# Kernel optimization log

Hardware: AMD Instinct MI355X
Metric: run time of the kernel (lower is better)

Reference implementation:

```python
import jax, jax.numpy as jnp
import numpy as np

B, D_IN, H1, H2, A = 8192, 512, 4096, 4096, 64
QMIN, QMAX = -128.0, 127.0  # int8 saturation range


def _int_vals(key, shape, spread):
    # integer-valued fixed-point tensor stored as float32
    return jnp.clip(jnp.round(jax.random.normal(key, shape) * spread), QMIN * spread, QMAX * spread).astype(jnp.float32)


def setup_inputs() -> dict:
    key = jax.random.key(0)
    ks = jax.random.split(key, 9)
    x = jnp.clip(jnp.round(jax.random.normal(ks[0], (B, D_IN)) * 32.0), QMIN, QMAX).astype(jnp.float32)
    w1 = jnp.clip(jnp.round(jax.random.normal(ks[1], (H1, D_IN)) * 16.0), QMIN, QMAX).astype(jnp.float32)
    b1 = _int_vals(ks[2], (H1,), 256.0)
    w2 = jnp.clip(jnp.round(jax.random.normal(ks[3], (H2, H1)) * 16.0), QMIN, QMAX).astype(jnp.float32)
    b2 = _int_vals(ks[4], (H2,), 256.0)
    w_mu = jnp.clip(jnp.round(jax.random.normal(ks[5], (A, H2)) * 16.0), QMIN, QMAX).astype(jnp.float32)
    b_mu = _int_vals(ks[6], (A,), 256.0)
    w_prob = jnp.clip(jnp.round(jax.random.normal(ks[7], (A, H2)) * 16.0), QMIN, QMAX).astype(jnp.float32)
    b_prob = _int_vals(ks[8], (A,), 256.0)
    M = jnp.full((1,), 2.0 ** -10, dtype=jnp.float32)  # per-layer requant multiplier
    s = jnp.full((1,), 0.05, dtype=jnp.float32)        # activation quantize scale
    return {
        "x": x, "w1": w1, "b1": b1, "w2": w2, "b2": b2,
        "w_mu": w_mu, "b_mu": b_mu, "w_prob": w_prob, "b_prob": b_prob,
        "M1": M, "M2": M, "M_mu": M, "M_prob": M,
        "s2": s, "s_mu": s, "s_prob": s,
    }


def _qlinear(x, w, b, M):
    # genesys fixed-point linear: int accumulate then requantize by multiplier M
    acc = jnp.matmul(x, w.T) + b  # integer-valued fp32 accumulator
    return jnp.round(M * acc)


def _quantize(src, scale, zero_point=0.0):
    return jnp.clip(jnp.round(src / scale) + zero_point, QMIN, QMAX)


def reference(x, w1, b1, w2, b2, w_mu, b_mu, w_prob, b_prob, M1, M2, M_mu, M_prob, s2, s_mu, s_prob):
    h = jax.nn.relu(_qlinear(x, w1, b1, M1))
    h = _quantize(h, s2)
    h = jax.nn.relu(_qlinear(h, w2, b2, M2))
    # NOTE: original forward_int feeds the un-quantized relu output into the
    # heads (x_mu/x_prob quantizations are dead code) and returns only prob.
    prob = _qlinear(h, w_prob, b_prob, M_prob)
    return prob
```

## Files before the change

kernel.cpp:

```cpp
#include <hip/hip_runtime.h>
#include <stdint.h>

#define NB   8192
#define DIN  512
#define NH1  4096
#define NH2  4096
#define NA   64

typedef int v4i __attribute__((ext_vector_type(4)));

__device__ __forceinline__ v4i mfma_i8(v4i a, v4i b, v4i c) {
    return __builtin_amdgcn_mfma_i32_16x16x64_i8(a, b, c, 0, 0, 0);
}

__device__ __forceinline__ void gload16(const void* g, const void* l) {
    __builtin_amdgcn_global_load_lds(
        (const __attribute__((address_space(1))) void*)(uintptr_t)g,
        (__attribute__((address_space(3))) void*)(uint32_t)(uintptr_t)l,
        16, 0, 0);
}

__global__ __launch_bounds__(256)
void prep(const float* __restrict__ x,  const float* __restrict__ w1,
          const float* __restrict__ w2, const float* __restrict__ wp,
          signed char* __restrict__ xf, signed char* __restrict__ w1_i8,
          signed char* __restrict__ w2_i8, signed char* __restrict__ wp_i8,
          int* __restrict__ S)
{
    __shared__ int red[256];
    const int b   = blockIdx.x;
    const int tid = threadIdx.x;

    if (b < 18432) {
        const float* in  = (b < 16384) ? w2 : w1;
        signed char* out = (b < 16384) ? w2_i8 : w1_i8;
        const int i = ((b < 16384) ? b : (b - 16384)) * 256 + tid;
        const float4 v = ((const float4*)in)[i];
        char4 c;
        c.x = (signed char)__float2int_rn(v.x);
        c.y = (signed char)__float2int_rn(v.y);
        c.z = (signed char)__float2int_rn(v.z);
        c.w = (signed char)__float2int_rn(v.w);
        ((char4*)out)[i] = c;
    } else if (b < 19456) {
        const int u   = (b - 18432) * 256 + tid;
        const int g   = u >> 9;
        const int kt  = (u >> 6) & 7;
        const int l   = u & 63;
        const int row = g * 16 + (l & 15);
        const int k0  = kt * 64 + (l >> 4) * 16;
        const float4* src = (const float4*)(x + (size_t)row * DIN + k0);
        signed char v[16];
        #pragma unroll
        for (int q = 0; q < 4; ++q) {
            const float4 f = src[q];
            v[q*4+0] = (signed char)__float2int_rn(f.x);
            v[q*4+1] = (signed char)__float2int_rn(f.y);
            v[q*4+2] = (signed char)__float2int_rn(f.z);
            v[q*4+3] = (signed char)__float2int_rn(f.w);
        }
        *(int4*)(xf + (size_t)u * 16) = *(const int4*)v;
    } else if (b < 19712) {
        const int i = (b - 19456) * 256 + tid;
        const float4 v = ((const float4*)wp)[i];
        char4 c;
        c.x = (signed char)__float2int_rn(v.x);
        c.y = (signed char)__float2int_rn(v.y);
        c.z = (signed char)__float2int_rn(v.z);
        c.w = (signed char)__float2int_rn(v.w);
        ((char4*)wp_i8)[i] = c;
    } else {
        const int a = b - 19712;
        int p = 0;
        for (int k = tid; k < NH2; k += 256) p += __float2int_rn(wp[(size_t)a * NH2 + k]);
        red[tid] = p; __syncthreads();
        for (int s = 128; s > 0; s >>= 1) { if (tid < s) red[tid] += red[tid + s]; __syncthreads(); }
        if (tid == 0) S[a] = red[0];
    }
}

template <int EPI>
__global__ __launch_bounds__(512, 4)
void gemm_af(const signed char* __restrict__ Af,
             const signed char* __restrict__ Bg,
             int M, int N, int K,
             const float* __restrict__ bias,
             const float* __restrict__ Mscale,
             const float* __restrict__ qscale,
             signed char* __restrict__ out0,
             signed char* __restrict__ out1)
{
    __shared__ __align__(16) signed char lds[69632];

    const int tid  = threadIdx.x;
    const int lane = tid & 63;
    const int wid  = tid >> 6;
    const int wm   = wid >> 1, wn = wid & 1;

    const int nwg  = gridDim.x;
    const int bid  = blockIdx.x;
    const int swzb = (bid & 7) * (nwg >> 3) + (bid >> 3);
    const int nbx  = N >> 7;
    const int bx   = swzb % nbx;
    const int by   = swzb / nbx;
    const int bm0  = by << 8, bn0 = bx << 7;

    const int srow = tid >> 2;
    const int sc   = (((tid & 3) ^ ((tid >> 3) & 3)) << 4);
    const signed char* bS = Bg + (size_t)(bn0 + srow) * K + sc;

    const int r    = lane & 15;
    const int pc   = (((lane >> 4) ^ ((r >> 1) & 3)) << 4);
    const int boff = wn * 4096 + r * 64 + pc;

    const int NKT = K >> 6;
    const signed char* afB = Af + (((size_t)((bm0 >> 4) + wm * 4) * NKT) << 10) + lane * 16;

    const int nt = K >> 6;

    v4i af[4], bf[4];
    #pragma unroll
    for (int m = 0; m < 4; ++m)
        af[m] = *(const v4i*)(afB + (((size_t)(m * NKT)) << 10));
    gload16(bS,      lds + tid * 16);
    gload16(bS + 64, lds + 8192 + tid * 16);
    asm volatile("s_waitcnt vmcnt(1)" ::: "memory");
    __builtin_amdgcn_s_barrier();

    v4i acc[4][4] = {};

    for (int t = 0; t < nt; ++t) {
        const signed char* L = lds + (t % 3) * 8192;
        #pragma unroll
        for (int n = 0; n < 4; ++n) bf[n] = *(const v4i*)(L + boff + n * 1024);

        const size_t tl = (size_t)((t + 1 < nt) ? (t + 1) : t);

        __builtin_amdgcn_s_setprio(1);
        #pragma unroll
        for (int m = 0; m < 4; ++m) {
            #pragma unroll
            for (int n = 0; n < 4; ++n)
                acc[m][n] = mfma_i8(af[m], bf[n], acc[m][n]);
            af[m] = *(const v4i*)(afB + (((size_t)(m * NKT) + tl) << 10));
        }
        __builtin_amdgcn_s_setprio(0);

        if (t + 2 < nt) {
            gload16(bS + ((t + 2) << 6), lds + ((t + 2) % 3) * 8192 + tid * 16);
            asm volatile("s_waitcnt vmcnt(1)" ::: "memory");
        } else if (t + 1 < nt) {
            asm volatile("s_waitcnt vmcnt(0)" ::: "memory");
        }
        __builtin_amdgcn_s_barrier();
    }

    __syncthreads();
    signed char* img0 = lds;
    signed char* img1 = lds + 34816;
    const int rowb = wm * 64 + ((lane >> 4) << 2);
    const int colb = wn * 64 + (lane & 15);

    if constexpr (EPI == 1) {
        const float Mv = Mscale[0];
        const float sv = qscale[0];
        #pragma unroll
        for (int n = 0; n < 4; ++n) {
            const int col  = colb + n * 16;
            const int bint = __float2int_rn(bias[bn0 + col]);
            #pragma unroll
            for (int m = 0; m < 4; ++m) {
                #pragma unroll
                for (int j = 0; j < 4; ++j) {
                    const int row  = rowb + m * 16 + j;
                    const int accv = acc[m][n][j] + bint;
                    float h = rintf(Mv * (float)accv);
                    h = fmaxf(h, 0.0f);
                    float q = rintf(h / sv);
                    q = fminf(fmaxf(q, -128.0f), 127.0f);
                    img0[row * 136 + col] = (signed char)(int)q;
                }
            }
        }
        __syncthreads();
        const int oNKT = N >> 6;
        #pragma unroll
        for (int i = 0; i < 4; ++i) {
            const int u    = i * 512 + tid;
            const int g_l  = u >> 7;
            const int kt_l = (u >> 6) & 1;
            const int l    = u & 63;
            const int lrow = g_l * 16 + (l & 15);
            const int lcol = kt_l * 64 + (l >> 4) * 16;
            const size_t g  = (size_t)((bm0 >> 4) + g_l);
            const size_t kt = (size_t)((bn0 >> 6) + kt_l);
            *(int4*)(out0 + ((g * oNKT + kt) << 10) + l * 16) =
                *(const int4*)(img0 + lrow * 136 + lcol);
        }
    } else {
        const float Mv = Mscale[0];
        #pragma unroll
        for (int n = 0; n < 4; ++n) {
            const int col  = colb + n * 16;
            const int bint = __float2int_rn(bias[bn0 + col]);
            #pragma unroll
            for (int m = 0; m < 4; ++m) {
                #pragma unroll
                for (int j = 0; j < 4; ++j) {
                    const int row  = rowb + m * 16 + j;
                    const int accv = acc[m][n][j] + bint;
                    double rr = rint((double)Mv * (double)accv);
                    rr = rr > 0.0 ? rr : 0.0;
                    const int v = (int)rr;
                    img0[row * 136 + col] = (signed char)((v & 255) - 128);
                    img1[row * 136 + col] = (signed char)((v >> 8) - 128);
                }
            }
        }
        __syncthreads();
        #pragma unroll
        for (int p = 0; p < 8; ++p) {
            const int idx = p * 512 + tid;
            const int row = idx >> 4;
            const int cb  = (idx & 15) * 8;
            const size_t gaddr = (size_t)(bm0 + row) * N + bn0 + cb;
            *(int2*)(out0 + gaddr) = *(const int2*)(img0 + row * 136 + cb);
            *(int2*)(out1 + gaddr) = *(const int2*)(img1 + row * 136 + cb);
        }
    }
}

__global__ __launch_bounds__(512, 1)
void head_mfma(const signed char* __restrict__ lo,
               const signed char* __restrict__ hi,
               const signed char* __restrict__ wpq,
               int* __restrict__ part)
{
    __shared__ __align__(16) signed char Bl[32768];
    __shared__ __align__(16) signed char Al[3][32768];

    const int tid  = threadIdx.x;
    const int lane = tid & 63;
    const int wid  = tid >> 6;
    const int rblk = blockIdx.x >> 3;
    const int kblk = blockIdx.x & 7;
    const int bm0  = rblk << 8;
    const int kb   = kblk << 9;

    #pragma unroll
    for (int s = 0; s < 4; ++s) {
        const int brow = s * 16 + (tid >> 5);
        const int pch  = tid & 31;
        const int lc   = pch ^ (brow & 7);
        gload16(wpq + (size_t)brow * NH2 + kb + lc * 16, Bl + brow * 512 + pch * 16);
    }

    const int srow  = tid >> 2;
    const int sclog = (tid & 3) ^ ((tid >> 3) & 3);
    const size_t ab = (size_t)(bm0 + srow) * NH2 + kb + sclog * 16;
    const size_t rK = (size_t)128 * NH2;

    #define HSTAGE(bp, ko) do { \
        gload16(lo + ab + (ko),      &Al[bp][0]     + tid * 16); \
        gload16(lo + ab + rK + (ko), &Al[bp][8192]  + tid * 16); \
        gload16(hi + ab + (ko),      &Al[bp][16384] + tid * 16); \
        gload16(hi + ab + rK + (ko), &Al[bp][24576] + tid * 16); } while (0)

    HSTAGE(0, 0);
    HSTAGE(1, 64);

    const int r    = lane & 15;
    const int cg   = lane >> 4;
    const int pcA  = (cg ^ ((r >> 1) & 3)) * 16;
    const int aoff = wid * 2048 + r * 64 + pcA;

    v4i accL[2][4] = {}, accH[2][4] = {};
    int cur = 0, nxt = 2;

    for (int t = 0; t < 8; ++t) {
        if (t < 7) asm volatile("s_waitcnt vmcnt(4)" ::: "memory");
        else       asm volatile("s_waitcnt vmcnt(0)" ::: "memory");
        __builtin_amdgcn_s_barrier();

        const signed char* A = &Al[cur][0];
        v4i bf[4], al[2], ah[2];
        #pragma unroll
        for (int n = 0; n < 4; ++n)
            bf[n] = *(const v4i*)(Bl + (n * 16 + r) * 512 + (((t * 4 + cg) ^ (r & 7)) * 16));
        #pragma unroll
        for (int m = 0; m < 2; ++m) al[m] = *(const v4i*)(A + aoff + m * 1024);
        #pragma unroll
        for (int m = 0; m < 2; ++m) ah[m] = *(const v4i*)(A + 16384 + aoff + m * 1024);

        if (t + 2 < 8) HSTAGE(nxt, (t + 2) << 6);

        __builtin_amdgcn_s_setprio(1);
        #pragma unroll
        for (int m = 0; m < 2; ++m)
            #pragma unroll
            for (int n = 0; n < 4; ++n) {
                accL[m][n] = mfma_i8(al[m], bf[n], accL[m][n]);
                accH[m][n] = mfma_i8(ah[m], bf[n], accH[m][n]);
            }
        __builtin_amdgcn_s_setprio(0);
        __builtin_amdgcn_s_barrier();

        cur = (cur == 2) ? 0 : cur + 1;
        nxt = (nxt == 2) ? 0 : nxt + 1;
    }
    #undef HSTAGE

    int* pb = part + (size_t)kblk * (NB * NA);
    const int rowb = bm0 + wid * 32 + ((lane >> 4) << 2);
    #pragma unroll
    for (int m = 0; m < 2; ++m)
        #pragma unroll
        for (int n = 0; n < 4; ++n) {
            const int a = n * 16 + (lane & 15);
            #pragma unroll
            for (int j = 0; j < 4; ++j) {
                const int row = rowb + m * 16 + j;
                pb[(size_t)row * NA + a] = accL[m][n][j] + (accH[m][n][j] << 8);
            }
        }
}

__global__ __launch_bounds__(256)
void comb_head(const int* __restrict__ part, const int* __restrict__ S,
               const float* __restrict__ bp, const float* __restrict__ Mp,
               float* __restrict__ out)
{
    const int t = blockIdx.x * 256 + threadIdx.x;
    const int a = t & 63;
    long long sum = 0;
    #pragma unroll
    for (int c = 0; c < 8; ++c) sum += part[(size_t)c * (NB * NA) + t];
    sum += 32896LL * (long long)S[a] + (long long)__float2int_rn(bp[a]);
    out[t] = (float)rint((double)Mp[0] * (double)sum);
}

extern "C" void kernel_launch(void* const* d_in, const int* in_sizes, int n_in,
                              void* d_out, int out_size, void* d_ws, size_t ws_size,
                              hipStream_t stream) {
    const float* x  = (const float*)d_in[0];
    const float* w1 = (const float*)d_in[1];
    const float* b1 = (const float*)d_in[2];
    const float* w2 = (const float*)d_in[3];
    const float* b2 = (const float*)d_in[4];
    const float* wp = (const float*)d_in[7];
    const float* bp = (const float*)d_in[8];
    const float* M1 = (const float*)d_in[9];
    const float* M2 = (const float*)d_in[10];
    const float* Mp = (const float*)d_in[12];
    const float* s2 = (const float*)d_in[13];

    const size_t MB = (size_t)1 << 20;
    char* ws = (char*)d_ws;
    signed char* xf    = (signed char*)(ws);
    signed char* w1_i8 = (signed char*)(ws + 4  * MB);
    signed char* w2_i8 = (signed char*)(ws + 6  * MB);
    signed char* wp_i8 = (signed char*)(ws + 22 * MB);
    int*         Ssum  = (int*)        (ws + 22 * MB + 512 * 1024);
    signed char* h1f   = (signed char*)(ws + 23 * MB);
    signed char* h2lo  = (signed char*)(ws + 55 * MB);
    signed char* h2hi  = (signed char*)(ws + 87 * MB);
    int*         part  = (int*)        (ws);

    prep<<<dim3(19776), dim3(256), 0, stream>>>(x, w1, w2, wp, xf, w1_i8, w2_i8, wp_i8, Ssum);

    gemm_af<1><<<dim3((NB / 256) * (NH1 / 128)), dim3(512), 0, stream>>>(
        xf, w1_i8, NB, NH1, DIN, b1, M1, s2, h1f, nullptr);
    gemm_af<2><<<dim3((NB / 256) * (NH2 / 128)), dim3(512), 0, stream>>>(
        h1f, w2_i8, NB, NH2, NH1, b2, M2, nullptr, h2lo, h2hi);
    head_mfma<<<dim3(256), dim3(512), 0, stream>>>(h2lo, h2hi, wp_i8, part);
    comb_head<<<dim3(NB * NA / 256), dim3(256), 0, stream>>>(part, Ssum, bp, Mp, (float*)d_out);
}
```

Before: 200.8 us.

## Pre-swizzle weights into MFMA fragment layout and load B directly from global

The prep kernel now writes w1 and w2 in the same per-lane MFMA fragment layout already used for activations. The GEMM then loads both A and B fragments straight from global memory into registers, dropping the LDS triple-buffer, the global_load_lds path and the per-iteration barriers. This removes LDS traffic and synchronisation from the main loop. In exchange it loses the explicit software prefetch and B-tile sharing through LDS, so each wave fetches its own B fragments from global or cache and memory latency must be hidden by occupancy and unroll-by-2.

```diff
diff --git a/kernel.cpp b/kernel.cpp
--- a/kernel.cpp
+++ b/kernel.cpp
@@ -20,48 +20,45 @@
         16, 0, 0);
 }
 
+__device__ __forceinline__ void frag_unit(const float* __restrict__ in, signed char* __restrict__ out,
+                                          int u, int K, int ktmask, int gshift) {
+    const int g   = u >> gshift;
+    const int kt  = (u >> 6) & ktmask;
+    const int l   = u & 63;
+    const int row = g * 16 + (l & 15);
+    const int k0  = kt * 64 + (l >> 4) * 16;
+    const float4* src = (const float4*)(in + (size_t)row * K + k0);
+    signed char v[16];
+    #pragma unroll
+    for (int q = 0; q < 4; ++q) {
+        const float4 f = src[q];
+        v[q*4+0] = (signed char)__float2int_rn(f.x);
+        v[q*4+1] = (signed char)__float2int_rn(f.y);
+        v[q*4+2] = (signed char)__float2int_rn(f.z);
+        v[q*4+3] = (signed char)__float2int_rn(f.w);
+    }
+    *(int4*)(out + (size_t)u * 16) = *(const int4*)v;
+}
+
 __global__ __launch_bounds__(256)
 void prep(const float* __restrict__ x,  const float* __restrict__ w1,
           const float* __restrict__ w2, const float* __restrict__ wp,
-          signed char* __restrict__ xf, signed char* __restrict__ w1_i8,
-          signed char* __restrict__ w2_i8, signed char* __restrict__ wp_i8,
+          signed char* __restrict__ xf, signed char* __restrict__ w1f,
+          signed char* __restrict__ w2f, signed char* __restrict__ wp_i8,
           int* __restrict__ S)
 {
     __shared__ int red[256];
     const int b   = blockIdx.x;
     const int tid = threadIdx.x;
 
-    if (b < 18432) {
-        const float* in  = (b < 16384) ? w2 : w1;
-        signed char* out = (b < 16384) ? w2_i8 : w1_i8;
-        const int i = ((b < 16384) ? b : (b - 16384)) * 256 + tid;
-        const float4 v = ((const float4*)in)[i];
-        char4 c;
-        c.x = (signed char)__float2int_rn(v.x);
-        c.y = (signed char)__float2int_rn(v.y);
-        c.z = (signed char)__float2int_rn(v.z);
-        c.w = (signed char)__float2int_rn(v.w);
-        ((char4*)out)[i] = c;
-    } else if (b < 19456) {
-        const int u   = (b - 18432) * 256 + tid;
-        const int g   = u >> 9;
-        const int kt  = (u >> 6) & 7;
-        const int l   = u & 63;
-        const int row = g * 16 + (l & 15);
-        const int k0  = kt * 64 + (l >> 4) * 16;
-        const float4* src = (const float4*)(x + (size_t)row * DIN + k0);
-        signed char v[16];
-        #pragma unroll
-        for (int q = 0; q < 4; ++q) {
-            const float4 f = src[q];
-            v[q*4+0] = (signed char)__float2int_rn(f.x);
-            v[q*4+1] = (signed char)__float2int_rn(f.y);
-            v[q*4+2] = (signed char)__float2int_rn(f.z);
-            v[q*4+3] = (signed char)__float2int_rn(f.w);
-        }
-        *(int4*)(xf + (size_t)u * 16) = *(const int4*)v;
-    } else if (b < 19712) {
-        const int i = (b - 19456) * 256 + tid;
+    if (b < 4096) {
+        frag_unit(w2, w2f, b * 256 + tid, NH1, 63, 12);
+    } else if (b < 4608) {
+        frag_unit(w1, w1f, (b - 4096) * 256 + tid, DIN, 7, 9);
+    } else if (b < 5632) {
+        frag_unit(x, xf, (b - 4608) * 256 + tid, DIN, 7, 9);
+    } else if (b < 5888) {
+        const int i = (b - 5632) * 256 + tid;
         const float4 v = ((const float4*)wp)[i];
         char4 c;
         c.x = (signed char)__float2int_rn(v.x);
@@ -70,7 +67,7 @@
         c.w = (signed char)__float2int_rn(v.w);
         ((char4*)wp_i8)[i] = c;
     } else {
-        const int a = b - 19712;
+        const int a = b - 5888;
         int p = 0;
         for (int k = tid; k < NH2; k += 256) p += __float2int_rn(wp[(size_t)a * NH2 + k]);
         red[tid] = p; __syncthreads();
@@ -81,8 +78,8 @@
 
 template <int EPI>
 __global__ __launch_bounds__(512, 4)
-void gemm_af(const signed char* __restrict__ Af,
-             const signed char* __restrict__ Bg,
+void gemm_ff(const signed char* __restrict__ Af,
+             const signed char* __restrict__ Bf,
              int M, int N, int K,
              const float* __restrict__ bias,
              const float* __restrict__ Mscale,
@@ -105,57 +102,31 @@
     const int by   = swzb / nbx;
     const int bm0  = by << 8, bn0 = bx << 7;
 
-    const int srow = tid >> 2;
-    const int sc   = (((tid & 3) ^ ((tid >> 3) & 3)) << 4);
-    const signed char* bS = Bg + (size_t)(bn0 + srow) * K + sc;
-
-    const int r    = lane & 15;
-    const int pc   = (((lane >> 4) ^ ((r >> 1) & 3)) << 4);
-    const int boff = wn * 4096 + r * 64 + pc;
-
     const int NKT = K >> 6;
-    const signed char* afB = Af + (((size_t)((bm0 >> 4) + wm * 4) * NKT) << 10) + lane * 16;
-
-    const int nt = K >> 6;
-
-    v4i af[4], bf[4];
-    #pragma unroll
-    for (int m = 0; m < 4; ++m)
-        af[m] = *(const v4i*)(afB + (((size_t)(m * NKT)) << 10));
-    gload16(bS,      lds + tid * 16);
-    gload16(bS + 64, lds + 8192 + tid * 16);
-    asm volatile("s_waitcnt vmcnt(1)" ::: "memory");
-    __builtin_amdgcn_s_barrier();
+    const signed char* afBase = Af + (((size_t)((bm0 >> 4) + wm * 4) * NKT) << 10) + lane * 16;
+    const signed char* bfBase = Bf + (((size_t)((bn0 >> 4) + wn * 4) * NKT) << 10) + lane * 16;
 
     v4i acc[4][4] = {};
 
-    for (int t = 0; t < nt; ++t) {
-        const signed char* L = lds + (t % 3) * 8192;
-        #pragma unroll
-        for (int n = 0; n < 4; ++n) bf[n] = *(const v4i*)(L + boff + n * 1024);
-
-        const size_t tl = (size_t)((t + 1 < nt) ? (t + 1) : t);
+    #pragma unroll 2
+    for (int t = 0; t < NKT; ++t) {
+        v4i af[4], bf[4];
+        #pragma unroll
+        for (int m = 0; m < 4; ++m)
+            af[m] = *(const v4i*)(afBase + ((size_t)(m * NKT + t) << 10));
+        #pragma unroll
+        for (int n = 0; n < 4; ++n)
+            bf[n] = *(const v4i*)(bfBase + ((size_t)(n * NKT + t) << 10));
 
         __builtin_amdgcn_s_setprio(1);
         #pragma unroll
-        for (int m = 0; m < 4; ++m) {
+        for (int m = 0; m < 4; ++m)
             #pragma unroll
             for (int n = 0; n < 4; ++n)
                 acc[m][n] = mfma_i8(af[m], bf[n], acc[m][n]);
-            af[m] = *(const v4i*)(afB + (((size_t)(m * NKT) + tl) << 10));
-        }
         __builtin_amdgcn_s_setprio(0);
-
-        if (t + 2 < nt) {
-            gload16(bS + ((t + 2) << 6), lds + ((t + 2) % 3) * 8192 + tid * 16);
-            asm volatile("s_waitcnt vmcnt(1)" ::: "memory");
-        } else if (t + 1 < nt) {
-            asm volatile("s_waitcnt vmcnt(0)" ::: "memory");
-        }
-        __builtin_amdgcn_s_barrier();
-    }
-
-    __syncthreads();
+    }
+
     signed char* img0 = lds;
     signed char* img1 = lds + 34816;
     const int rowb = wm * 64 + ((lane >> 4) << 2);
@@ -357,8 +328,8 @@
     const size_t MB = (size_t)1 << 20;
     char* ws = (char*)d_ws;
     signed char* xf    = (signed char*)(ws);
-    signed char* w1_i8 = (signed char*)(ws + 4  * MB);
-    signed char* w2_i8 = (signed char*)(ws + 6  * MB);
+    signed char* w1f   = (signed char*)(ws + 4  * MB);
+    signed char* w2f   = (signed char*)(ws + 6  * MB);
     signed char* wp_i8 = (signed char*)(ws + 22 * MB);
     int*         Ssum  = (int*)        (ws + 22 * MB + 512 * 1024);
     signed char* h1f   = (signed char*)(ws + 23 * MB);
@@ -366,12 +337,12 @@
     signed char* h2hi  = (signed char*)(ws + 87 * MB);
     int*         part  = (int*)        (ws);
 
-    prep<<<dim3(19776), dim3(256), 0, stream>>>(x, w1, w2, wp, xf, w1_i8, w2_i8, wp_i8, Ssum);
-
-    gemm_af<1><<<dim3((NB / 256) * (NH1 / 128)), dim3(512), 0, stream>>>(
-        xf, w1_i8, NB, NH1, DIN, b1, M1, s2, h1f, nullptr);
-    gemm_af<2><<<dim3((NB / 256) * (NH2 / 128)), dim3(512), 0, stream>>>(
-        h1f, w2_i8, NB, NH2, NH1, b2, M2, nullptr, h2lo, h2hi);
+    prep<<<dim3(5952), dim3(256), 0, stream>>>(x, w1, w2, wp, xf, w1f, w2f, wp_i8, Ssum);
+
+    gemm_ff<1><<<dim3((NB / 256) * (NH1 / 128)), dim3(512), 0, stream>>>(
+        xf, w1f, NB, NH1, DIN, b1, M1, s2, h1f, nullptr);
+    gemm_ff<2><<<dim3((NB / 256) * (NH2 / 128)), dim3(512), 0, stream>>>(
+        h1f, w2f, NB, NH2, NH1, b2, M2, nullptr, h2lo, h2hi);
     head_mfma<<<dim3(256), dim3(512), 0, stream>>>(h2lo, h2hi, wp_i8, part);
     comb_head<<<dim3(NB * NA / 256), dim3(256), 0, stream>>>(part, Ssum, bp, Mp, (float*)d_out);
 }
```

After: 239.6 us. 1.19x slower.
